# Kernel tuning notes

Hardware: AMD Instinct MI355X
Metric: run time of the kernel (lower is better)

## Reference

```python
import jax, jax.numpy as jnp
import numpy as np

B, H, NQ, NL, NA = 262144, 256, 4, 2, 16


def _apply_1q(s, U, q):
    # s: [B, 2,2,2,2]; U: [B,2,2] (batched) or [2,2] (shared)
    s = jnp.moveaxis(s, 1 + q, -1)
    if U.ndim == 3:
        s = jnp.einsum('bij,b...j->b...i', U, s)
    else:
        s = jnp.einsum('ij,b...j->b...i', U, s)
    return jnp.moveaxis(s, -1, 1 + q)


def _apply_cnot(s, c, t):
    s = jnp.moveaxis(s, (1 + c, 1 + t), (-2, -1))
    s = jnp.stack([s[..., 0, :], s[..., 1, ::-1]], axis=-2)  # flip target when control=1
    return jnp.moveaxis(s, (-2, -1), (1 + c, 1 + t))


def _rx(theta):
    # batched RX: theta [B] -> [B,2,2]
    c = jnp.cos(theta / 2).astype(jnp.complex64)
    s = (-1j) * jnp.sin(theta / 2)
    return jnp.stack([jnp.stack([c, s], -1), jnp.stack([s, c], -1)], -2)


def _rot(phi, theta, omega):
    # PennyLane Rot = RZ(omega) @ RY(theta) @ RZ(phi), scalar angles -> [2,2]
    c, s = jnp.cos(theta / 2), jnp.sin(theta / 2)
    return jnp.array(1, jnp.complex64) * jnp.stack([
        jnp.stack([jnp.exp(-0.5j * (phi + omega)) * c, -jnp.exp(0.5j * (phi - omega)) * s], -1),
        jnp.stack([jnp.exp(-0.5j * (phi - omega)) * s, jnp.exp(0.5j * (phi + omega)) * c], -1),
    ], -2)


def _circuit(angles, q_weights):
    # angles: [B, NQ] -> PauliZ expvals [B, NQ] via 4-qubit state-vector sim
    b = angles.shape[0]
    s = jnp.zeros((b,) + (2,) * NQ, jnp.complex64)
    s = s.at[(slice(None),) + (0,) * NQ].set(1.0)
    for q in range(NQ):  # AngleEmbedding (RX rotations)
        s = _apply_1q(s, _rx(angles[:, q]), q)
    for l in range(NL):  # StronglyEntanglingLayers
        for w in range(NQ):
            s = _apply_1q(s, _rot(q_weights[l, w, 0], q_weights[l, w, 1], q_weights[l, w, 2]), w)
        r = l % (NQ - 1) + 1
        for w in range(NQ):
            s = _apply_cnot(s, w, (w + r) % NQ)
    probs = s.real ** 2 + s.imag ** 2  # [B,2,2,2,2]
    zs = []
    axes = tuple(range(1, NQ + 1))
    for q in range(NQ):
        p = probs.sum(tuple(a for a in axes if a != 1 + q))  # [B,2]
        zs.append(p[:, 0] - p[:, 1])
    return jnp.stack(zs, axis=1)


def setup_inputs() -> dict:
    key = jax.random.key(0)
    ks = jax.random.split(key, 6)
    return {
        'h': jax.random.normal(ks[0], (B, H), jnp.float32),
        'W_embed': jax.random.normal(ks[1], (NQ, H), jnp.float32) / np.sqrt(H),
        'b_embed': jnp.zeros((NQ,), jnp.float32),
        'q_weights': jax.random.uniform(ks[2], (NL, NQ, 3), jnp.float32, 0.0, 2 * np.pi),
        'W_out': jax.random.normal(ks[3], (NA, NQ), jnp.float32) / np.sqrt(NQ),
        'b_out': jnp.zeros((NA,), jnp.float32),
    }


def reference(h, W_embed, b_embed, q_weights, W_out, b_out):
    angles = jnp.tanh(h @ W_embed.T + b_embed)  # [B, NQ]
    z = _circuit(angles, q_weights)             # [B, NQ]
    return z @ W_out.T + b_out                  # [B, NA]
```

## Files before the change

### kernel.cpp

```cpp
#include <hip/hip_runtime.h>

#define NQ 4
#define NL 2
#define NA 16
#define HDIM 256
#define RPB 256

template<int M>
__device__ __forceinline__ void apply_u(float* sr, float* si, const float* u) {
    const float u00r = u[0], u00i = u[1], u01r = u[2], u01i = u[3];
    const float u10r = u[4], u10i = u[5], u11r = u[6], u11i = u[7];
#pragma unroll
    for (int k = 0; k < 16; ++k) {
        if (k & M) continue;
        const int k1 = k | M;
        const float a0r = sr[k],  a0i = si[k];
        const float a1r = sr[k1], a1i = si[k1];
        sr[k]  = u00r*a0r - u00i*a0i + u01r*a1r - u01i*a1i;
        si[k]  = u00r*a0i + u00i*a0r + u01r*a1i + u01i*a1r;
        sr[k1] = u10r*a0r - u10i*a0i + u11r*a1r - u11i*a1i;
        si[k1] = u10r*a0i + u10i*a0r + u11r*a1i + u11i*a1r;
    }
}

template<int MC, int MT>
__device__ __forceinline__ void cnot(float* sr, float* si) {
#pragma unroll
    for (int k = 0; k < 16; ++k) {
        if ((k & MC) && !(k & MT)) {
            const int k1 = k | MT;
            float tr = sr[k]; sr[k] = sr[k1]; sr[k1] = tr;
            float ti = si[k]; si[k] = si[k1]; si[k1] = ti;
        }
    }
}

__global__ __launch_bounds__(256) void qph_kernel(
    const float* __restrict__ h,
    const float* __restrict__ W_embed,
    const float* __restrict__ b_embed,
    const float* __restrict__ q_weights,
    const float* __restrict__ W_out,
    const float* __restrict__ b_out,
    float* __restrict__ out,
    int B)
{
    __shared__ __align__(16) float w_lds[NQ * HDIM];
    __shared__ float rot_lds[NL * NQ][8];
    __shared__ float wout_lds[NA * NQ];
    __shared__ float bout_lds[NA];

    const int tid = threadIdx.x;
    const long rowBase = (long)blockIdx.x * RPB;

#pragma unroll
    for (int k = 0; k < 4; ++k) w_lds[tid + k * 256] = W_embed[tid + k * 256];
    if (tid < NA * NQ) wout_lds[tid] = W_out[tid];
    if (tid < NA)      bout_lds[tid] = b_out[tid];
    if (tid < NL * NQ) {
        const float phi = q_weights[tid * 3 + 0];
        const float th  = q_weights[tid * 3 + 1];
        const float om  = q_weights[tid * 3 + 2];
        const float c  = cosf(0.5f * th), s  = sinf(0.5f * th);
        const float al = 0.5f * (phi + om), be = 0.5f * (phi - om);
        const float ca = cosf(al), sa = sinf(al);
        const float cb = cosf(be), sb = sinf(be);
        rot_lds[tid][0] =  ca * c;  rot_lds[tid][1] = -sa * c;
        rot_lds[tid][2] = -cb * s;  rot_lds[tid][3] = -sb * s;
        rot_lds[tid][4] =  cb * s;  rot_lds[tid][5] = -sb * s;
        rot_lds[tid][6] =  ca * c;  rot_lds[tid][7] =  sa * c;
    }
    __syncthreads();

    const int t = tid & 3;
    const int g = tid >> 2;
    const float be0 = b_embed[0], be1 = b_embed[1], be2 = b_embed[2], be3 = b_embed[3];

    float my0 = 0.f, my1 = 0.f, my2 = 0.f, my3 = 0.f;

#pragma unroll
    for (int rr = 0; rr < 4; ++rr) {
        const int  lrow = g * 4 + rr;
        const long grow = rowBase + lrow;
        float acc0 = 0.f, acc1 = 0.f, acc2 = 0.f, acc3 = 0.f;
        if (grow < B) {
            const float4* hrow = (const float4*)(h + grow * (long)HDIM);
#pragma unroll
            for (int j = 0; j < 16; ++j) {
                const float4 hv = hrow[j * 4 + t];
                const float4 w0 = *(const float4*)&w_lds[0 * HDIM + j * 16 + t * 4];
                const float4 w1 = *(const float4*)&w_lds[1 * HDIM + j * 16 + t * 4];
                const float4 w2 = *(const float4*)&w_lds[2 * HDIM + j * 16 + t * 4];
                const float4 w3 = *(const float4*)&w_lds[3 * HDIM + j * 16 + t * 4];
                acc0 = fmaf(hv.x, w0.x, fmaf(hv.y, w0.y, fmaf(hv.z, w0.z, fmaf(hv.w, w0.w, acc0))));
                acc1 = fmaf(hv.x, w1.x, fmaf(hv.y, w1.y, fmaf(hv.z, w1.z, fmaf(hv.w, w1.w, acc1))));
                acc2 = fmaf(hv.x, w2.x, fmaf(hv.y, w2.y, fmaf(hv.z, w2.z, fmaf(hv.w, w2.w, acc2))));
                acc3 = fmaf(hv.x, w3.x, fmaf(hv.y, w3.y, fmaf(hv.z, w3.z, fmaf(hv.w, w3.w, acc3))));
            }
        }
        acc0 += __shfl_xor(acc0, 1); acc0 += __shfl_xor(acc0, 2);
        acc1 += __shfl_xor(acc1, 1); acc1 += __shfl_xor(acc1, 2);
        acc2 += __shfl_xor(acc2, 1); acc2 += __shfl_xor(acc2, 2);
        acc3 += __shfl_xor(acc3, 1); acc3 += __shfl_xor(acc3, 2);
        if (t == rr) { my0 = acc0; my1 = acc1; my2 = acc2; my3 = acc3; }
    }

    const long grow = rowBase + tid;
    if (grow >= B) return;

    const float ang0 = tanhf(my0 + be0);
    const float ang1 = tanhf(my1 + be1);
    const float ang2 = tanhf(my2 + be2);
    const float ang3 = tanhf(my3 + be3);

    float sr[16], si[16];
#pragma unroll
    for (int k = 0; k < 16; ++k) { sr[k] = 0.f; si[k] = 0.f; }
    sr[0] = 1.0f;

    const float angs[4] = {ang0, ang1, ang2, ang3};
#pragma unroll
    for (int q = 0; q < NQ; ++q) {
        const float th = angs[q];
        const float c = __cosf(0.5f * th), s = __sinf(0.5f * th);
        const int m = 8 >> q;
#pragma unroll
        for (int k = 0; k < 16; ++k) {
            if (k & m) continue;
            const int k1 = k | m;
            const float a0r = sr[k],  a0i = si[k];
            const float a1r = sr[k1], a1i = si[k1];
            sr[k]  = c * a0r + s * a1i;
            si[k]  = c * a0i - s * a1r;
            sr[k1] = s * a0i + c * a1r;
            si[k1] = c * a1i - s * a0r;
        }
    }

    apply_u<8>(sr, si, rot_lds[0]);
    apply_u<4>(sr, si, rot_lds[1]);
    apply_u<2>(sr, si, rot_lds[2]);
    apply_u<1>(sr, si, rot_lds[3]);
    cnot<8, 4>(sr, si);
    cnot<4, 2>(sr, si);
    cnot<2, 1>(sr, si);
    cnot<1, 8>(sr, si);
    apply_u<8>(sr, si, rot_lds[4]);
    apply_u<4>(sr, si, rot_lds[5]);
    apply_u<2>(sr, si, rot_lds[6]);
    apply_u<1>(sr, si, rot_lds[7]);
    cnot<8, 2>(sr, si);
    cnot<4, 1>(sr, si);
    cnot<2, 8>(sr, si);
    cnot<1, 4>(sr, si);

    float p[16];
#pragma unroll
    for (int k = 0; k < 16; ++k) p[k] = sr[k] * sr[k] + si[k] * si[k];
    float z[4];
#pragma unroll
    for (int q = 0; q < NQ; ++q) {
        const int m = 8 >> q;
        float zz = 0.f;
#pragma unroll
        for (int k = 0; k < 16; ++k) zz += (k & m) ? -p[k] : p[k];
        z[q] = zz;
    }

    float4* out4 = (float4*)(out + grow * (long)NA);
#pragma unroll
    for (int i = 0; i < 4; ++i) {
        float o[4];
#pragma unroll
        for (int jj = 0; jj < 4; ++jj) {
            const int a = i * 4 + jj;
            float v = bout_lds[a];
#pragma unroll
            for (int q = 0; q < NQ; ++q) v = fmaf(z[q], wout_lds[a * 4 + q], v);
            o[jj] = v;
        }
        out4[i] = make_float4(o[0], o[1], o[2], o[3]);
    }
}

extern "C" void kernel_launch(void* const* d_in, const int* in_sizes, int n_in,
                              void* d_out, int out_size, void* d_ws, size_t ws_size,
                              hipStream_t stream) {
    const float* h         = (const float*)d_in[0];
    const float* W_embed   = (const float*)d_in[1];
    const float* b_embed   = (const float*)d_in[2];
    const float* q_weights = (const float*)d_in[3];
    const float* W_out     = (const float*)d_in[4];
    const float* b_out     = (const float*)d_in[5];
    float* out = (float*)d_out;

    const int B = in_sizes[0] / HDIM;
    const int blocks = (B + RPB - 1) / RPB;
    qph_kernel<<<blocks, 256, 0, stream>>>(h, W_embed, b_embed, q_weights, W_out, b_out, out, B);
}
```

Measured before the change: 56.71 us.

## Keep W_embed in registers, use 16-lane row reduction and LDS z staging

Each thread now holds its slice of W_embed in registers, so the per-iteration LDS reads of the embedding weights go away. The row-to-thread mapping changes so that 16 lanes cooperate on each row with contiguous float4 loads, and partial sums are reduced with ds_swizzle. The circuit's z values are staged through LDS so that the output writes keep row-contiguous thread order. This adds 64 registers per thread for the weights, occupancy is constrained to 4 blocks via launch bounds, and an extra __syncthreads is introduced.

```diff
diff --git a/kernel.cpp b/kernel.cpp
--- a/kernel.cpp
+++ b/kernel.cpp
@@ -6,20 +6,27 @@
 #define HDIM 256
 #define RPB 256
 
+template<int PATTERN>
+__device__ __forceinline__ float swz_add(float x) {
+    return x + __int_as_float(__builtin_amdgcn_ds_swizzle(__float_as_int(x), PATTERN));
+}
+
+__device__ __forceinline__ float dot4(float4 a, float4 b) {
+    return fmaf(a.x, b.x, fmaf(a.y, b.y, fmaf(a.z, b.z, a.w * b.w)));
+}
+
 template<int M>
-__device__ __forceinline__ void apply_u(float* sr, float* si, const float* u) {
-    const float u00r = u[0], u00i = u[1], u01r = u[2], u01i = u[3];
-    const float u10r = u[4], u10i = u[5], u11r = u[6], u11i = u[7];
+__device__ __forceinline__ void apply_u(float* sr, float* si, const float4 u0, const float4 u1) {
 #pragma unroll
     for (int k = 0; k < 16; ++k) {
         if (k & M) continue;
         const int k1 = k | M;
         const float a0r = sr[k],  a0i = si[k];
         const float a1r = sr[k1], a1i = si[k1];
-        sr[k]  = u00r*a0r - u00i*a0i + u01r*a1r - u01i*a1i;
-        si[k]  = u00r*a0i + u00i*a0r + u01r*a1i + u01i*a1r;
-        sr[k1] = u10r*a0r - u10i*a0i + u11r*a1r - u11i*a1i;
-        si[k1] = u10r*a0i + u10i*a0r + u11r*a1i + u11i*a1r;
+        sr[k]  = u0.x*a0r - u0.y*a0i + u0.z*a1r - u0.w*a1i;
+        si[k]  = u0.x*a0i + u0.y*a0r + u0.z*a1i + u0.w*a1r;
+        sr[k1] = u1.x*a0r - u1.y*a0i + u1.z*a1r - u1.w*a1i;
+        si[k1] = u1.x*a0i + u1.y*a0r + u1.z*a1i + u1.w*a1r;
     }
 }
 
@@ -35,7 +42,7 @@
     }
 }
 
-__global__ __launch_bounds__(256) void qph_kernel(
+__global__ __launch_bounds__(256, 4) void qph_kernel(
     const float* __restrict__ h,
     const float* __restrict__ W_embed,
     const float* __restrict__ b_embed,
@@ -45,16 +52,16 @@
     float* __restrict__ out,
     int B)
 {
-    __shared__ __align__(16) float w_lds[NQ * HDIM];
-    __shared__ float rot_lds[NL * NQ][8];
-    __shared__ float wout_lds[NA * NQ];
+    __shared__ __align__(16) float rot_lds[NL * NQ][8];
+    __shared__ __align__(16) float wout_lds[NA * NQ];
     __shared__ float bout_lds[NA];
+    __shared__ __align__(16) float zbuf[RPB][4];
 
     const int tid = threadIdx.x;
+    const int l16 = tid & 15;
+    const int g   = tid >> 4;
     const long rowBase = (long)blockIdx.x * RPB;
 
-#pragma unroll
-    for (int k = 0; k < 4; ++k) w_lds[tid + k * 256] = W_embed[tid + k * 256];
     if (tid < NA * NQ) wout_lds[tid] = W_out[tid];
     if (tid < NA)      bout_lds[tid] = b_out[tid];
     if (tid < NL * NQ) {
@@ -72,112 +79,133 @@
     }
     __syncthreads();
 
-    const int t = tid & 3;
-    const int g = tid >> 2;
+    float4 wreg[4][4];
+#pragma unroll
+    for (int q = 0; q < 4; ++q)
+#pragma unroll
+        for (int s = 0; s < 4; ++s)
+            wreg[q][s] = *(const float4*)(W_embed + q * HDIM + s * 64 + l16 * 4);
     const float be0 = b_embed[0], be1 = b_embed[1], be2 = b_embed[2], be3 = b_embed[3];
 
     float my0 = 0.f, my1 = 0.f, my2 = 0.f, my3 = 0.f;
 
 #pragma unroll
-    for (int rr = 0; rr < 4; ++rr) {
-        const int  lrow = g * 4 + rr;
-        const long grow = rowBase + lrow;
-        float acc0 = 0.f, acc1 = 0.f, acc2 = 0.f, acc3 = 0.f;
-        if (grow < B) {
-            const float4* hrow = (const float4*)(h + grow * (long)HDIM);
-#pragma unroll
-            for (int j = 0; j < 16; ++j) {
-                const float4 hv = hrow[j * 4 + t];
-                const float4 w0 = *(const float4*)&w_lds[0 * HDIM + j * 16 + t * 4];
-                const float4 w1 = *(const float4*)&w_lds[1 * HDIM + j * 16 + t * 4];
-                const float4 w2 = *(const float4*)&w_lds[2 * HDIM + j * 16 + t * 4];
-                const float4 w3 = *(const float4*)&w_lds[3 * HDIM + j * 16 + t * 4];
-                acc0 = fmaf(hv.x, w0.x, fmaf(hv.y, w0.y, fmaf(hv.z, w0.z, fmaf(hv.w, w0.w, acc0))));
-                acc1 = fmaf(hv.x, w1.x, fmaf(hv.y, w1.y, fmaf(hv.z, w1.z, fmaf(hv.w, w1.w, acc1))));
-                acc2 = fmaf(hv.x, w2.x, fmaf(hv.y, w2.y, fmaf(hv.z, w2.z, fmaf(hv.w, w2.w, acc2))));
-                acc3 = fmaf(hv.x, w3.x, fmaf(hv.y, w3.y, fmaf(hv.z, w3.z, fmaf(hv.w, w3.w, acc3))));
+    for (int it = 0; it < 16; ++it) {
+        const long r = rowBase + it * 16 + g;
+        float4 hv0 = make_float4(0,0,0,0), hv1 = hv0, hv2 = hv0, hv3 = hv0;
+        if (r < B) {
+            const float4* hrow = (const float4*)(h + r * (long)HDIM);
+            hv0 = hrow[0 * 16 + l16];
+            hv1 = hrow[1 * 16 + l16];
+            hv2 = hrow[2 * 16 + l16];
+            hv3 = hrow[3 * 16 + l16];
+        }
+        float a[4];
+#pragma unroll
+        for (int q = 0; q < 4; ++q) {
+            a[q] = dot4(hv0, wreg[q][0]) + dot4(hv1, wreg[q][1])
+                 + dot4(hv2, wreg[q][2]) + dot4(hv3, wreg[q][3]);
+        }
+#pragma unroll
+        for (int q = 0; q < 4; ++q) {
+            a[q] = swz_add<0x041F>(a[q]);
+            a[q] = swz_add<0x081F>(a[q]);
+            a[q] = swz_add<0x101F>(a[q]);
+            a[q] = swz_add<0x201F>(a[q]);
+        }
+        if (l16 == it) { my0 = a[0]; my1 = a[1]; my2 = a[2]; my3 = a[3]; }
+    }
+
+    const int  lrow = l16 * 16 + g;
+    const long grow = rowBase + lrow;
+
+    if (grow < B) {
+        const float angs[4] = {tanhf(my0 + be0), tanhf(my1 + be1),
+                               tanhf(my2 + be2), tanhf(my3 + be3)};
+
+        float sr[16], si[16];
+#pragma unroll
+        for (int k = 0; k < 16; ++k) { sr[k] = 0.f; si[k] = 0.f; }
+        sr[0] = 1.0f;
+
+#pragma unroll
+        for (int q = 0; q < NQ; ++q) {
+            const float th = angs[q];
+            const float c = __cosf(0.5f * th), s = __sinf(0.5f * th);
+            const int m = 8 >> q;
+#pragma unroll
+            for (int k = 0; k < 16; ++k) {
+                if (k & m) continue;
+                const int k1 = k | m;
+                const float a0r = sr[k],  a0i = si[k];
+                const float a1r = sr[k1], a1i = si[k1];
+                sr[k]  = c * a0r + s * a1i;
+                si[k]  = c * a0i - s * a1r;
+                sr[k1] = s * a0i + c * a1r;
+                si[k1] = c * a1i - s * a0r;
             }
         }
-        acc0 += __shfl_xor(acc0, 1); acc0 += __shfl_xor(acc0, 2);
-        acc1 += __shfl_xor(acc1, 1); acc1 += __shfl_xor(acc1, 2);
-        acc2 += __shfl_xor(acc2, 1); acc2 += __shfl_xor(acc2, 2);
-        acc3 += __shfl_xor(acc3, 1); acc3 += __shfl_xor(acc3, 2);
-        if (t == rr) { my0 = acc0; my1 = acc1; my2 = acc2; my3 = acc3; }
-    }
-
-    const long grow = rowBase + tid;
-    if (grow >= B) return;
-
-    const float ang0 = tanhf(my0 + be0);
-    const float ang1 = tanhf(my1 + be1);
-    const float ang2 = tanhf(my2 + be2);
-    const float ang3 = tanhf(my3 + be3);
-
-    float sr[16], si[16];
-#pragma unroll
-    for (int k = 0; k < 16; ++k) { sr[k] = 0.f; si[k] = 0.f; }
-    sr[0] = 1.0f;
-
-    const float angs[4] = {ang0, ang1, ang2, ang3};
-#pragma unroll
-    for (int q = 0; q < NQ; ++q) {
-        const float th = angs[q];
-        const float c = __cosf(0.5f * th), s = __sinf(0.5f * th);
-        const int m = 8 >> q;
-#pragma unroll
-        for (int k = 0; k < 16; ++k) {
-            if (k & m) continue;
-            const int k1 = k | m;
-            const float a0r = sr[k],  a0i = si[k];
-            const float a1r = sr[k1], a1i = si[k1];
-            sr[k]  = c * a0r + s * a1i;
-            si[k]  = c * a0i - s * a1r;
-            sr[k1] = s * a0i + c * a1r;
-            si[k1] = c * a1i - s * a0r;
-        }
-    }
-
-    apply_u<8>(sr, si, rot_lds[0]);
-    apply_u<4>(sr, si, rot_lds[1]);
-    apply_u<2>(sr, si, rot_lds[2]);
-    apply_u<1>(sr, si, rot_lds[3]);
-    cnot<8, 4>(sr, si);
-    cnot<4, 2>(sr, si);
-    cnot<2, 1>(sr, si);
-    cnot<1, 8>(sr, si);
-    apply_u<8>(sr, si, rot_lds[4]);
-    apply_u<4>(sr, si, rot_lds[5]);
-    apply_u<2>(sr, si, rot_lds[6]);
-    apply_u<1>(sr, si, rot_lds[7]);
-    cnot<8, 2>(sr, si);
-    cnot<4, 1>(sr, si);
-    cnot<2, 8>(sr, si);
-    cnot<1, 4>(sr, si);
-
-    float p[16];
-#pragma unroll
-    for (int k = 0; k < 16; ++k) p[k] = sr[k] * sr[k] + si[k] * si[k];
-    float z[4];
-#pragma unroll
-    for (int q = 0; q < NQ; ++q) {
-        const int m = 8 >> q;
-        float zz = 0.f;
-#pragma unroll
-        for (int k = 0; k < 16; ++k) zz += (k & m) ? -p[k] : p[k];
-        z[q] = zz;
-    }
-
-    float4* out4 = (float4*)(out + grow * (long)NA);
+
+#pragma unroll
+        for (int w = 0; w < 4; ++w) {
+            const float4 u0 = *(const float4*)&rot_lds[w][0];
+            const float4 u1 = *(const float4*)&rot_lds[w][4];
+            if (w == 0) apply_u<8>(sr, si, u0, u1);
+            if (w == 1) apply_u<4>(sr, si, u0, u1);
+            if (w == 2) apply_u<2>(sr, si, u0, u1);
+            if (w == 3) apply_u<1>(sr, si, u0, u1);
+        }
+        cnot<8, 4>(sr, si);
+        cnot<4, 2>(sr, si);
+        cnot<2, 1>(sr, si);
+        cnot<1, 8>(sr, si);
+#pragma unroll
+        for (int w = 0; w < 4; ++w) {
+            const float4 u0 = *(const float4*)&rot_lds[4 + w][0];
+            const float4 u1 = *(const float4*)&rot_lds[4 + w][4];
+            if (w == 0) apply_u<8>(sr, si, u0, u1);
+            if (w == 1) apply_u<4>(sr, si, u0, u1);
+            if (w == 2) apply_u<2>(sr, si, u0, u1);
+            if (w == 3) apply_u<1>(sr, si, u0, u1);
+        }
+        cnot<8, 2>(sr, si);
+        cnot<4, 1>(sr, si);
+        cnot<2, 8>(sr, si);
+        cnot<1, 4>(sr, si);
+
+        float p[16];
+#pragma unroll
+        for (int k = 0; k < 16; ++k) p[k] = sr[k] * sr[k] + si[k] * si[k];
+        float4 z;
+        {
+            float zt[4];
+#pragma unroll
+            for (int q = 0; q < NQ; ++q) {
+                const int m = 8 >> q;
+                float zz = 0.f;
+#pragma unroll
+                for (int k = 0; k < 16; ++k) zz += (k & m) ? -p[k] : p[k];
+                zt[q] = zz;
+            }
+            z = make_float4(zt[0], zt[1], zt[2], zt[3]);
+        }
+        *(float4*)&zbuf[lrow][0] = z;
+    }
+    __syncthreads();
+
+    const long orow = rowBase + tid;
+    if (orow >= B) return;
+    const float4 zv = *(const float4*)&zbuf[tid][0];
+
+    float4* out4 = (float4*)(out + orow * (long)NA);
 #pragma unroll
     for (int i = 0; i < 4; ++i) {
         float o[4];
 #pragma unroll
         for (int jj = 0; jj < 4; ++jj) {
             const int a = i * 4 + jj;
-            float v = bout_lds[a];
-#pragma unroll
-            for (int q = 0; q < NQ; ++q) v = fmaf(z[q], wout_lds[a * 4 + q], v);
-            o[jj] = v;
+            const float4 w = *(const float4*)&wout_lds[a * 4];
+            o[jj] = bout_lds[a] + zv.x * w.x + zv.y * w.y + zv.z * w.z + zv.w * w.w;
         }
         out4[i] = make_float4(o[0], o[1], o[2], o[3]);
     }
```

After: 110.9 us. +95.5%, slower.
